# Optimization experiments

Hardware: AMD Instinct MI355X
Metric: run time of the kernel (lower is better)

Reference implementation:

```python
import jax, jax.numpy as jnp
import numpy as np

N_CELLS = 500_000
B = 512
D_X = 128
D_Z = 32
D_IN = D_X + D_Z  # 160
H = 256
D_OUT = 16


def _linear_params(key, fan_in, fan_out):
    k1, k2 = jax.random.split(key)
    bound = 1.0 / np.sqrt(fan_in)
    W = jax.random.uniform(k1, (fan_in, fan_out), jnp.float32, -bound, bound)
    b = jax.random.uniform(k2, (fan_out,), jnp.float32, -bound, bound)
    return W, b


def setup_inputs() -> dict:
    key = jax.random.key(0)
    ks = jax.random.split(key, 8)
    X = jax.random.uniform(ks[0], (N_CELLS, D_X), jnp.float32)  # nonneg counts-like
    Z = jax.random.normal(ks[1], (B, D_Z), jnp.float32)
    cell_to_batch = jax.random.randint(ks[2], (N_CELLS,), 0, B, jnp.int64)
    sample_idx_batch = jnp.arange(B, dtype=jnp.int64)
    W1, b1 = _linear_params(ks[3], D_IN, H)
    W2, b2 = _linear_params(ks[4], H, H)
    W3, b3 = _linear_params(ks[5], H, D_OUT)
    return {"X": X, "Z": Z, "W1": W1, "b1": b1, "W2": W2, "b2": b2,
            "W3": W3, "b3": b3, "cell_to_batch": cell_to_batch,
            "sample_idx_batch": sample_idx_batch}


def reference(X, Z, W1, b1, W2, b2, W3, b3, cell_to_batch, sample_idx_batch):
    # gather per-sample covariates to per-cell rows
    Zc = Z[cell_to_batch]                              # [N, D_Z]
    seg = sample_idx_batch[cell_to_batch]              # [N] remapped sample ids
    # preprocessor: log-normalize X, concat covariates
    Xp = jnp.concatenate([jnp.log1p(X), Zc], axis=-1)  # [N, D_IN]
    # cell predictor MLP (Linear-ReLU x2 + Linear)
    h = jax.nn.relu(Xp @ W1 + b1)
    h = jax.nn.relu(h @ W2 + b2)
    X_cell = h @ W3 + b3                               # [N, D_OUT]
    # aggregator: segment mean over cells of each sample
    nseg = sample_idx_batch.shape[0]
    sums = jax.ops.segment_sum(X_cell, seg, num_segments=nseg)
    counts = jax.ops.segment_sum(jnp.ones((X_cell.shape[0], 1), X_cell.dtype), seg, num_segments=nseg)
    Y_sample = sums / jnp.maximum(counts, 1.0)
    # postprocessor: identity
    return Y_sample
```

## Files before the change

kernel.cpp:

```cpp
#include <hip/hip_runtime.h>
#include <hip/hip_bf16.h>

typedef __attribute__((ext_vector_type(8))) short short8;
typedef __attribute__((ext_vector_type(4))) float floatx4;

#define N_CELLS  500000
#define B_SAMP   512
#define D_X      128
#define D_Z      32
#define D_IN     160
#define H_DIM    256
#define D_OUT    16

#define M_TILE   32
#define LDA      168
#define LDH      264

#define NREP     64

#define OFF_W1P   0
#define OFF_W2P   81920
#define OFF_W3P   212992
#define OFF_ACC   221184
#define OFF_CNT   2318336

__global__ void pack_w(const float* __restrict__ W, __hip_bfloat16* __restrict__ dst,
                       int N, int kS) {
    int idx = blockIdx.x * blockDim.x + threadIdx.x;
    int j = idx & 7;
    int L = (idx >> 3) & 63;
    int s = (idx >> 9) % kS;
    int t = idx / (kS << 9);
    int k = s * 32 + ((L >> 4) << 3) + j;
    int n = t * 16 + (L & 15);
    dst[idx] = __float2bfloat16(W[(size_t)k * N + n]);
}

__global__ void zero_ws(float* __restrict__ p, int n) {
    int i = blockIdx.x * blockDim.x + threadIdx.x;
    if (i < n) p[i] = 0.0f;
}

__global__ __launch_bounds__(256, 3)
void fused_mlp(const float* __restrict__ X, const float* __restrict__ Z,
               const int* __restrict__ c2b, const int* __restrict__ sidx,
               const float* __restrict__ b1, const float* __restrict__ b2,
               const float* __restrict__ b3,
               const __hip_bfloat16* __restrict__ w1p,
               const __hip_bfloat16* __restrict__ w2p,
               const __hip_bfloat16* __restrict__ w3p,
               float* __restrict__ accs, float* __restrict__ cnts) {
    __shared__ __hip_bfloat16 sXp[M_TILE][LDA];
    __shared__ __hip_bfloat16 sH[2][M_TILE][LDH];
    __shared__ float sP[4][M_TILE][D_OUT];

    const int tid = threadIdx.x;
    const int w   = tid >> 6;
    const int L   = tid & 63;
    const int q   = L >> 4;
    const int ln  = L & 15;
    const int base = blockIdx.x * M_TILE;

#pragma unroll
    for (int i = 0; i < 4; ++i) {
        int idx = tid + i * 256;
        int row = idx >> 5;
        int c4  = idx & 31;
        float4 v = *(const float4*)(X + (size_t)(base + row) * D_X + c4 * 4);
        __hip_bfloat16* d = &sXp[row][c4 * 4];
        d[0] = __float2bfloat16(__logf(1.0f + v.x));
        d[1] = __float2bfloat16(__logf(1.0f + v.y));
        d[2] = __float2bfloat16(__logf(1.0f + v.z));
        d[3] = __float2bfloat16(__logf(1.0f + v.w));
    }
    {
        int row = tid >> 3;
        int c0  = (tid & 7) * 4;
        int b   = c2b[base + row];
        float4 v = *(const float4*)(Z + (size_t)b * D_Z + c0);
        __hip_bfloat16* d = &sXp[row][D_X + c0];
        d[0] = __float2bfloat16(v.x);
        d[1] = __float2bfloat16(v.y);
        d[2] = __float2bfloat16(v.z);
        d[3] = __float2bfloat16(v.w);
    }
    __syncthreads();

    floatx4 acc[2][4];
#pragma unroll
    for (int mt = 0; mt < 2; ++mt)
#pragma unroll
        for (int nt = 0; nt < 4; ++nt)
            acc[mt][nt] = (floatx4){0.f, 0.f, 0.f, 0.f};

    float bias1[4];
#pragma unroll
    for (int nt = 0; nt < 4; ++nt) bias1[nt] = b1[w * 64 + nt * 16 + ln];

#pragma unroll
    for (int s = 0; s < 5; ++s) {
        short8 a0 = *(const short8*)&sXp[ln][s * 32 + q * 8];
        short8 a1 = *(const short8*)&sXp[16 + ln][s * 32 + q * 8];
#pragma unroll
        for (int nt = 0; nt < 4; ++nt) {
            int t = w * 4 + nt;
            short8 bf = *(const short8*)(w1p + (size_t)(((t * 5 + s) << 6) + L) * 8);
            acc[0][nt] = __builtin_amdgcn_mfma_f32_16x16x32_bf16(a0, bf, acc[0][nt], 0, 0, 0);
            acc[1][nt] = __builtin_amdgcn_mfma_f32_16x16x32_bf16(a1, bf, acc[1][nt], 0, 0, 0);
        }
    }
#pragma unroll
    for (int mt = 0; mt < 2; ++mt)
#pragma unroll
        for (int nt = 0; nt < 4; ++nt)
#pragma unroll
            for (int r = 0; r < 4; ++r) {
                float v = fmaxf(acc[mt][nt][r] + bias1[nt], 0.0f);
                sH[0][mt * 16 + q * 4 + r][w * 64 + nt * 16 + ln] = __float2bfloat16(v);
            }
    __syncthreads();

#pragma unroll
    for (int mt = 0; mt < 2; ++mt)
#pragma unroll
        for (int nt = 0; nt < 4; ++nt)
            acc[mt][nt] = (floatx4){0.f, 0.f, 0.f, 0.f};

    float bias2[4];
#pragma unroll
    for (int nt = 0; nt < 4; ++nt) bias2[nt] = b2[w * 64 + nt * 16 + ln];

#pragma unroll
    for (int s = 0; s < 8; ++s) {
        short8 a0 = *(const short8*)&sH[0][ln][s * 32 + q * 8];
        short8 a1 = *(const short8*)&sH[0][16 + ln][s * 32 + q * 8];
#pragma unroll
        for (int nt = 0; nt < 4; ++nt) {
            int t = w * 4 + nt;
            short8 bf = *(const short8*)(w2p + (size_t)(((t * 8 + s) << 6) + L) * 8);
            acc[0][nt] = __builtin_amdgcn_mfma_f32_16x16x32_bf16(a0, bf, acc[0][nt], 0, 0, 0);
            acc[1][nt] = __builtin_amdgcn_mfma_f32_16x16x32_bf16(a1, bf, acc[1][nt], 0, 0, 0);
        }
    }
#pragma unroll
    for (int mt = 0; mt < 2; ++mt)
#pragma unroll
        for (int nt = 0; nt < 4; ++nt)
#pragma unroll
            for (int r = 0; r < 4; ++r) {
                float v = fmaxf(acc[mt][nt][r] + bias2[nt], 0.0f);
                sH[1][mt * 16 + q * 4 + r][w * 64 + nt * 16 + ln] = __float2bfloat16(v);
            }
    __syncthreads();

    floatx4 acc3[2];
    acc3[0] = (floatx4){0.f, 0.f, 0.f, 0.f};
    acc3[1] = (floatx4){0.f, 0.f, 0.f, 0.f};
#pragma unroll
    for (int ss = 0; ss < 2; ++ss) {
        int s = w * 2 + ss;
        short8 a0 = *(const short8*)&sH[1][ln][s * 32 + q * 8];
        short8 a1 = *(const short8*)&sH[1][16 + ln][s * 32 + q * 8];
        short8 bf = *(const short8*)(w3p + (size_t)((s << 6) + L) * 8);
        acc3[0] = __builtin_amdgcn_mfma_f32_16x16x32_bf16(a0, bf, acc3[0], 0, 0, 0);
        acc3[1] = __builtin_amdgcn_mfma_f32_16x16x32_bf16(a1, bf, acc3[1], 0, 0, 0);
    }
#pragma unroll
    for (int mt = 0; mt < 2; ++mt)
#pragma unroll
        for (int r = 0; r < 4; ++r)
            sP[w][mt * 16 + q * 4 + r][ln] = acc3[mt][r];
    __syncthreads();

    float* accR = accs + (size_t)(blockIdx.x & (NREP - 1)) * (B_SAMP * D_OUT);
    float* cntR = cnts + (size_t)(blockIdx.x & (NREP - 1)) * B_SAMP;
#pragma unroll
    for (int i = 0; i < 2; ++i) {
        int idx = tid + i * 256;
        int m = idx >> 4, n = idx & 15;
        float v = sP[0][m][n] + sP[1][m][n] + sP[2][m][n] + sP[3][m][n] + b3[n];
        int b = c2b[base + m];
        int s = sidx[b];
        atomicAdd(&accR[(size_t)s * D_OUT + n], v);
        if (n == 0) atomicAdd(&cntR[s], 1.0f);
    }
}

__global__ __launch_bounds__(256)
void finalize(const float* __restrict__ accs, const float* __restrict__ cnts,
              float* __restrict__ out) {
    int o = blockIdx.x * blockDim.x + threadIdx.x;
    int s = o >> 4;
    float sum = 0.f, cnt = 0.f;
#pragma unroll 8
    for (int r = 0; r < NREP; ++r) {
        sum += accs[(size_t)r * (B_SAMP * D_OUT) + o];
        cnt += cnts[(size_t)r * B_SAMP + s];
    }
    out[o] = sum / fmaxf(cnt, 1.0f);
}

extern "C" void kernel_launch(void* const* d_in, const int* in_sizes, int n_in,
                              void* d_out, int out_size, void* d_ws, size_t ws_size,
                              hipStream_t stream) {
    const float* X   = (const float*)d_in[0];
    const float* Z   = (const float*)d_in[1];
    const float* W1  = (const float*)d_in[2];
    const float* b1  = (const float*)d_in[3];
    const float* W2  = (const float*)d_in[4];
    const float* b2  = (const float*)d_in[5];
    const float* W3  = (const float*)d_in[6];
    const float* b3  = (const float*)d_in[7];
    const int*   c2b = (const int*)d_in[8];
    const int*   sidx= (const int*)d_in[9];

    char* ws = (char*)d_ws;
    __hip_bfloat16* w1p = (__hip_bfloat16*)(ws + OFF_W1P);
    __hip_bfloat16* w2p = (__hip_bfloat16*)(ws + OFF_W2P);
    __hip_bfloat16* w3p = (__hip_bfloat16*)(ws + OFF_W3P);
    float* accs = (float*)(ws + OFF_ACC);
    float* cnts = (float*)(ws + OFF_CNT);
    float* out  = (float*)d_out;

    {
        int nz = NREP * (B_SAMP * D_OUT + B_SAMP);
        zero_ws<<<(nz + 255) / 256, 256, 0, stream>>>(accs, nz);
    }

    pack_w<<<160, 256, 0, stream>>>(W1, w1p, H_DIM, 5);
    pack_w<<<256, 256, 0, stream>>>(W2, w2p, H_DIM, 8);
    pack_w<<<16,  256, 0, stream>>>(W3, w3p, D_OUT, 8);

    fused_mlp<<<N_CELLS / M_TILE, 256, 0, stream>>>(X, Z, c2b, sidx, b1, b2, b3,
                                                    w1p, w2p, w3p, accs, cnts);
    finalize<<<32, 256, 0, stream>>>(accs, cnts, out);
}
```

Before: 511.9 us.

## Enlarge MLP tile to 64 rows, transpose MFMA operands, fuse prep kernels

Each block now handles 64 cells with 512 threads in a 2x4 wave grid, which doubles reuse of every weight fragment loaded from global memory. The MFMA operands are swapped so each lane holds four consecutive output columns, allowing packed bf16 stores and bias-initialised accumulators. The ln(2) factor is folded into W1 so log2 can replace log. Layer 3 finishes in a single wave per 16 rows with no cross-wave partial-sum reduction, and the zeroing and three weight-packing launches are merged into one prep kernel. In exchange, LDS use per block and register pressure rise, which may lower occupancy, and a tail guard is added for the partial last tile.

```diff
diff --git a/kernel.cpp b/kernel.cpp
--- a/kernel.cpp
+++ b/kernel.cpp
@@ -2,6 +2,7 @@
 #include <hip/hip_bf16.h>
 
 typedef __attribute__((ext_vector_type(8))) short short8;
+typedef __attribute__((ext_vector_type(4))) short short4v;
 typedef __attribute__((ext_vector_type(4))) float floatx4;
 
 #define N_CELLS  500000
@@ -12,8 +13,8 @@
 #define H_DIM    256
 #define D_OUT    16
 
-#define M_TILE   32
-#define LDA      168
+#define M_TILE   64
+#define NBLK     7813
 #define LDH      264
 
 #define NREP     64
@@ -24,24 +25,50 @@
 #define OFF_ACC   221184
 #define OFF_CNT   2318336
 
-__global__ void pack_w(const float* __restrict__ W, __hip_bfloat16* __restrict__ dst,
-                       int N, int kS) {
-    int idx = blockIdx.x * blockDim.x + threadIdx.x;
+#define ZERO_BLKS 2176
+#define W1_BLKS   160
+#define W2_BLKS   256
+#define W3_BLKS   16
+
+__device__ __forceinline__ short bfb(float x) {
+    union { __hip_bfloat16 h; short s; } u;
+    u.h = __float2bfloat16(x);
+    return u.s;
+}
+
+__global__ __launch_bounds__(256)
+void prep(const float* __restrict__ W1, const float* __restrict__ W2,
+          const float* __restrict__ W3,
+          __hip_bfloat16* __restrict__ w1p, __hip_bfloat16* __restrict__ w2p,
+          __hip_bfloat16* __restrict__ w3p, float* __restrict__ accs) {
+    int bid = blockIdx.x;
+    if (bid < ZERO_BLKS) {
+        accs[bid * 256 + threadIdx.x] = 0.0f;
+        return;
+    }
+    const float* W; __hip_bfloat16* dst; int N, kS, idx, scaleK;
+    if (bid < ZERO_BLKS + W1_BLKS) {
+        idx = (bid - ZERO_BLKS) * 256 + threadIdx.x;
+        W = W1; dst = w1p; N = H_DIM; kS = 5; scaleK = 128;
+    } else if (bid < ZERO_BLKS + W1_BLKS + W2_BLKS) {
+        idx = (bid - ZERO_BLKS - W1_BLKS) * 256 + threadIdx.x;
+        W = W2; dst = w2p; N = H_DIM; kS = 8; scaleK = 0;
+    } else {
+        idx = (bid - ZERO_BLKS - W1_BLKS - W2_BLKS) * 256 + threadIdx.x;
+        W = W3; dst = w3p; N = D_OUT; kS = 8; scaleK = 0;
+    }
     int j = idx & 7;
     int L = (idx >> 3) & 63;
     int s = (idx >> 9) % kS;
     int t = idx / (kS << 9);
     int k = s * 32 + ((L >> 4) << 3) + j;
     int n = t * 16 + (L & 15);
-    dst[idx] = __float2bfloat16(W[(size_t)k * N + n]);
-}
-
-__global__ void zero_ws(float* __restrict__ p, int n) {
-    int i = blockIdx.x * blockDim.x + threadIdx.x;
-    if (i < n) p[i] = 0.0f;
-}
-
-__global__ __launch_bounds__(256, 3)
+    float v = W[(size_t)k * N + n];
+    if (k < scaleK) v *= 0.6931471805599453f;
+    dst[idx] = __float2bfloat16(v);
+}
+
+__global__ __launch_bounds__(512, 4)
 void fused_mlp(const float* __restrict__ X, const float* __restrict__ Z,
                const int* __restrict__ c2b, const int* __restrict__ sidx,
                const float* __restrict__ b1, const float* __restrict__ b2,
@@ -50,139 +77,129 @@
                const __hip_bfloat16* __restrict__ w2p,
                const __hip_bfloat16* __restrict__ w3p,
                float* __restrict__ accs, float* __restrict__ cnts) {
-    __shared__ __hip_bfloat16 sXp[M_TILE][LDA];
-    __shared__ __hip_bfloat16 sH[2][M_TILE][LDH];
-    __shared__ float sP[4][M_TILE][D_OUT];
+    __shared__ __hip_bfloat16 sA[M_TILE][LDH];
+    __shared__ __hip_bfloat16 sB[M_TILE][LDH];
 
     const int tid = threadIdx.x;
     const int w   = tid >> 6;
     const int L   = tid & 63;
     const int q   = L >> 4;
     const int ln  = L & 15;
+    const int wm  = w >> 2;
+    const int wn  = w & 3;
     const int base = blockIdx.x * M_TILE;
 
 #pragma unroll
     for (int i = 0; i < 4; ++i) {
-        int idx = tid + i * 256;
+        int idx = tid + i * 512;
         int row = idx >> 5;
         int c4  = idx & 31;
-        float4 v = *(const float4*)(X + (size_t)(base + row) * D_X + c4 * 4);
-        __hip_bfloat16* d = &sXp[row][c4 * 4];
-        d[0] = __float2bfloat16(__logf(1.0f + v.x));
-        d[1] = __float2bfloat16(__logf(1.0f + v.y));
-        d[2] = __float2bfloat16(__logf(1.0f + v.z));
-        d[3] = __float2bfloat16(__logf(1.0f + v.w));
+        int gr = base + row; if (gr >= N_CELLS) gr = N_CELLS - 1;
+        float4 v = *(const float4*)(X + (size_t)gr * D_X + c4 * 4);
+        short4v pk;
+        pk.x = bfb(__log2f(1.0f + v.x));
+        pk.y = bfb(__log2f(1.0f + v.y));
+        pk.z = bfb(__log2f(1.0f + v.z));
+        pk.w = bfb(__log2f(1.0f + v.w));
+        *(short4v*)&sA[row][c4 * 4] = pk;
     }
     {
         int row = tid >> 3;
         int c0  = (tid & 7) * 4;
-        int b   = c2b[base + row];
+        int gr = base + row; if (gr >= N_CELLS) gr = N_CELLS - 1;
+        int b  = c2b[gr];
         float4 v = *(const float4*)(Z + (size_t)b * D_Z + c0);
-        __hip_bfloat16* d = &sXp[row][D_X + c0];
-        d[0] = __float2bfloat16(v.x);
-        d[1] = __float2bfloat16(v.y);
-        d[2] = __float2bfloat16(v.z);
-        d[3] = __float2bfloat16(v.w);
+        short4v pk;
+        pk.x = bfb(v.x); pk.y = bfb(v.y); pk.z = bfb(v.z); pk.w = bfb(v.w);
+        *(short4v*)&sA[row][D_X + c0] = pk;
     }
     __syncthreads();
 
     floatx4 acc[2][4];
+
+#pragma unroll
+    for (int nt = 0; nt < 4; ++nt) {
+        float4 bv = *(const float4*)(b1 + wn * 64 + nt * 16 + q * 4);
+        acc[0][nt] = (floatx4){bv.x, bv.y, bv.z, bv.w};
+        acc[1][nt] = acc[0][nt];
+    }
+#pragma unroll
+    for (int s = 0; s < 5; ++s) {
+        short8 x0 = *(const short8*)&sA[wm * 32 + ln][s * 32 + q * 8];
+        short8 x1 = *(const short8*)&sA[wm * 32 + 16 + ln][s * 32 + q * 8];
+#pragma unroll
+        for (int nt = 0; nt < 4; ++nt) {
+            int t = wn * 4 + nt;
+            short8 wf = *(const short8*)(w1p + (size_t)(((t * 5 + s) << 6) + L) * 8);
+            acc[0][nt] = __builtin_amdgcn_mfma_f32_16x16x32_bf16(wf, x0, acc[0][nt], 0, 0, 0);
+            acc[1][nt] = __builtin_amdgcn_mfma_f32_16x16x32_bf16(wf, x1, acc[1][nt], 0, 0, 0);
+        }
+    }
 #pragma unroll
     for (int mt = 0; mt < 2; ++mt)
 #pragma unroll
-        for (int nt = 0; nt < 4; ++nt)
-            acc[mt][nt] = (floatx4){0.f, 0.f, 0.f, 0.f};
-
-    float bias1[4];
-#pragma unroll
-    for (int nt = 0; nt < 4; ++nt) bias1[nt] = b1[w * 64 + nt * 16 + ln];
-
-#pragma unroll
-    for (int s = 0; s < 5; ++s) {
-        short8 a0 = *(const short8*)&sXp[ln][s * 32 + q * 8];
-        short8 a1 = *(const short8*)&sXp[16 + ln][s * 32 + q * 8];
-#pragma unroll
-        for (int nt = 0; nt < 4; ++nt) {
-            int t = w * 4 + nt;
-            short8 bf = *(const short8*)(w1p + (size_t)(((t * 5 + s) << 6) + L) * 8);
-            acc[0][nt] = __builtin_amdgcn_mfma_f32_16x16x32_bf16(a0, bf, acc[0][nt], 0, 0, 0);
-            acc[1][nt] = __builtin_amdgcn_mfma_f32_16x16x32_bf16(a1, bf, acc[1][nt], 0, 0, 0);
+        for (int nt = 0; nt < 4; ++nt) {
+            short4v pk;
+            pk.x = bfb(fmaxf(acc[mt][nt][0], 0.0f));
+            pk.y = bfb(fmaxf(acc[mt][nt][1], 0.0f));
+            pk.z = bfb(fmaxf(acc[mt][nt][2], 0.0f));
+            pk.w = bfb(fmaxf(acc[mt][nt][3], 0.0f));
+            *(short4v*)&sB[wm * 32 + mt * 16 + ln][wn * 64 + nt * 16 + q * 4] = pk;
+        }
+    __syncthreads();
+
+#pragma unroll
+    for (int nt = 0; nt < 4; ++nt) {
+        float4 bv = *(const float4*)(b2 + wn * 64 + nt * 16 + q * 4);
+        acc[0][nt] = (floatx4){bv.x, bv.y, bv.z, bv.w};
+        acc[1][nt] = acc[0][nt];
+    }
+#pragma unroll
+    for (int s = 0; s < 8; ++s) {
+        short8 x0 = *(const short8*)&sB[wm * 32 + ln][s * 32 + q * 8];
+        short8 x1 = *(const short8*)&sB[wm * 32 + 16 + ln][s * 32 + q * 8];
+#pragma unroll
+        for (int nt = 0; nt < 4; ++nt) {
+            int t = wn * 4 + nt;
+            short8 wf = *(const short8*)(w2p + (size_t)(((t * 8 + s) << 6) + L) * 8);
+            acc[0][nt] = __builtin_amdgcn_mfma_f32_16x16x32_bf16(wf, x0, acc[0][nt], 0, 0, 0);
+            acc[1][nt] = __builtin_amdgcn_mfma_f32_16x16x32_bf16(wf, x1, acc[1][nt], 0, 0, 0);
         }
     }
 #pragma unroll
     for (int mt = 0; mt < 2; ++mt)
 #pragma unroll
-        for (int nt = 0; nt < 4; ++nt)
-#pragma unroll
-            for (int r = 0; r < 4; ++r) {
-                float v = fmaxf(acc[mt][nt][r] + bias1[nt], 0.0f);
-                sH[0][mt * 16 + q * 4 + r][w * 64 + nt * 16 + ln] = __float2bfloat16(v);
-            }
+        for (int nt = 0; nt < 4; ++nt) {
+            short4v pk;
+            pk.x = bfb(fmaxf(acc[mt][nt][0], 0.0f));
+            pk.y = bfb(fmaxf(acc[mt][nt][1], 0.0f));
+            pk.z = bfb(fmaxf(acc[mt][nt][2], 0.0f));
+            pk.w = bfb(fmaxf(acc[mt][nt][3], 0.0f));
+            *(short4v*)&sA[wm * 32 + mt * 16 + ln][wn * 64 + nt * 16 + q * 4] = pk;
+        }
     __syncthreads();
 
-#pragma unroll
-    for (int mt = 0; mt < 2; ++mt)
-#pragma unroll
-        for (int nt = 0; nt < 4; ++nt)
-            acc[mt][nt] = (floatx4){0.f, 0.f, 0.f, 0.f};
-
-    float bias2[4];
-#pragma unroll
-    for (int nt = 0; nt < 4; ++nt) bias2[nt] = b2[w * 64 + nt * 16 + ln];
-
-#pragma unroll
-    for (int s = 0; s < 8; ++s) {
-        short8 a0 = *(const short8*)&sH[0][ln][s * 32 + q * 8];
-        short8 a1 = *(const short8*)&sH[0][16 + ln][s * 32 + q * 8];
-#pragma unroll
-        for (int nt = 0; nt < 4; ++nt) {
-            int t = w * 4 + nt;
-            short8 bf = *(const short8*)(w2p + (size_t)(((t * 8 + s) << 6) + L) * 8);
-            acc[0][nt] = __builtin_amdgcn_mfma_f32_16x16x32_bf16(a0, bf, acc[0][nt], 0, 0, 0);
-            acc[1][nt] = __builtin_amdgcn_mfma_f32_16x16x32_bf16(a1, bf, acc[1][nt], 0, 0, 0);
-        }
-    }
-#pragma unroll
-    for (int mt = 0; mt < 2; ++mt)
-#pragma unroll
-        for (int nt = 0; nt < 4; ++nt)
-#pragma unroll
-            for (int r = 0; r < 4; ++r) {
-                float v = fmaxf(acc[mt][nt][r] + bias2[nt], 0.0f);
-                sH[1][mt * 16 + q * 4 + r][w * 64 + nt * 16 + ln] = __float2bfloat16(v);
-            }
-    __syncthreads();
-
-    floatx4 acc3[2];
-    acc3[0] = (floatx4){0.f, 0.f, 0.f, 0.f};
-    acc3[1] = (floatx4){0.f, 0.f, 0.f, 0.f};
-#pragma unroll
-    for (int ss = 0; ss < 2; ++ss) {
-        int s = w * 2 + ss;
-        short8 a0 = *(const short8*)&sH[1][ln][s * 32 + q * 8];
-        short8 a1 = *(const short8*)&sH[1][16 + ln][s * 32 + q * 8];
-        short8 bf = *(const short8*)(w3p + (size_t)((s << 6) + L) * 8);
-        acc3[0] = __builtin_amdgcn_mfma_f32_16x16x32_bf16(a0, bf, acc3[0], 0, 0, 0);
-        acc3[1] = __builtin_amdgcn_mfma_f32_16x16x32_bf16(a1, bf, acc3[1], 0, 0, 0);
-    }
-#pragma unroll
-    for (int mt = 0; mt < 2; ++mt)
-#pragma unroll
-        for (int r = 0; r < 4; ++r)
-            sP[w][mt * 16 + q * 4 + r][ln] = acc3[mt][r];
-    __syncthreads();
-
-    float* accR = accs + (size_t)(blockIdx.x & (NREP - 1)) * (B_SAMP * D_OUT);
-    float* cntR = cnts + (size_t)(blockIdx.x & (NREP - 1)) * B_SAMP;
-#pragma unroll
-    for (int i = 0; i < 2; ++i) {
-        int idx = tid + i * 256;
-        int m = idx >> 4, n = idx & 15;
-        float v = sP[0][m][n] + sP[1][m][n] + sP[2][m][n] + sP[3][m][n] + b3[n];
-        int b = c2b[base + m];
-        int s = sidx[b];
-        atomicAdd(&accR[(size_t)s * D_OUT + n], v);
-        if (n == 0) atomicAdd(&cntR[s], 1.0f);
+    if (w < 4) {
+        float4 bv = *(const float4*)(b3 + q * 4);
+        floatx4 a3 = (floatx4){bv.x, bv.y, bv.z, bv.w};
+#pragma unroll
+        for (int s = 0; s < 8; ++s) {
+            short8 h  = *(const short8*)&sA[w * 16 + ln][s * 32 + q * 8];
+            short8 wf = *(const short8*)(w3p + (size_t)((s << 6) + L) * 8);
+            a3 = __builtin_amdgcn_mfma_f32_16x16x32_bf16(wf, h, a3, 0, 0, 0);
+        }
+        int cell = base + w * 16 + ln;
+        if (cell < N_CELLS) {
+            int b = c2b[cell];
+            int so = sidx[b];
+            int rep = blockIdx.x & (NREP - 1);
+            float* dst = accs + (size_t)rep * (B_SAMP * D_OUT) + (size_t)so * D_OUT + q * 4;
+            atomicAdd(dst + 0, a3[0]);
+            atomicAdd(dst + 1, a3[1]);
+            atomicAdd(dst + 2, a3[2]);
+            atomicAdd(dst + 3, a3[3]);
+            if (q == 0) atomicAdd(cnts + (size_t)rep * B_SAMP + so, 1.0f);
+        }
     }
 }
 
@@ -222,16 +239,10 @@
     float* cnts = (float*)(ws + OFF_CNT);
     float* out  = (float*)d_out;
 
-    {
-        int nz = NREP * (B_SAMP * D_OUT + B_SAMP);
-        zero_ws<<<(nz + 255) / 256, 256, 0, stream>>>(accs, nz);
-    }
-
-    pack_w<<<160, 256, 0, stream>>>(W1, w1p, H_DIM, 5);
-    pack_w<<<256, 256, 0, stream>>>(W2, w2p, H_DIM, 8);
-    pack_w<<<16,  256, 0, stream>>>(W3, w3p, D_OUT, 8);
-
-    fused_mlp<<<N_CELLS / M_TILE, 256, 0, stream>>>(X, Z, c2b, sidx, b1, b2, b3,
-                                                    w1p, w2p, w3p, accs, cnts);
+    prep<<<ZERO_BLKS + W1_BLKS + W2_BLKS + W3_BLKS, 256, 0, stream>>>(
+        W1, W2, W3, w1p, w2p, w3p, accs);
+
+    fused_mlp<<<NBLK, 512, 0, stream>>>(X, Z, c2b, sidx, b1, b2, b3,
+                                        w1p, w2p, w3p, accs, cnts);
     finalize<<<32, 256, 0, stream>>>(accs, cnts, out);
 }
```

New measurement: 492.7 us. -3.8%, faster.
